# Optimization experiments

Measured on AMD Instinct MI355X. Metric: run time of the kernel, lower is better.

## Reference

```python
import jax, jax.numpy as jnp
import numpy as np

NUM_HEADS = 16
EMBED_DIM = 2048
HEAD_DIM = EMBED_DIM // NUM_HEADS
B, S = 2, 2048


def setup_inputs() -> dict:
    key = jax.random.key(0)
    ks = jax.random.split(key, 12)
    E = EMBED_DIM
    scale = 1.0 / np.sqrt(E)  # xavier-ish for square E->E dense
    inp = {
        "x": jax.random.normal(ks[0], (B, S, E), dtype=jnp.float32),
        "sin": jax.random.uniform(ks[1], (1, NUM_HEADS, S, HEAD_DIM), dtype=jnp.float32),
        "cos": jax.random.uniform(ks[2], (1, NUM_HEADS, S, HEAD_DIM), dtype=jnp.float32),
        "mask": jax.random.randint(ks[3], (B, S, S), 0, 2, dtype=jnp.int32),
        "Wq": jax.random.normal(ks[4], (E, E), dtype=jnp.float32) * scale,
        "bq": jnp.zeros((E,), dtype=jnp.float32),
        "Wk": jax.random.normal(ks[5], (E, E), dtype=jnp.float32) * scale,
        "bk": jnp.zeros((E,), dtype=jnp.float32),
        "Wv": jax.random.normal(ks[6], (E, E), dtype=jnp.float32) * scale,
        "bv": jnp.zeros((E,), dtype=jnp.float32),
        "Wo": jax.random.normal(ks[7], (E, E), dtype=jnp.float32) * scale,
        "bo": jnp.zeros((E,), dtype=jnp.float32),
    }
    return inp


def _minus_swap_alternate(t):
    # stack([-t[...,1::2], t[...,::2]], -1).reshape(t.shape)
    return jnp.stack([-t[..., 1::2], t[..., ::2]], axis=-1).reshape(t.shape)


def _forward(x, sin, cos, mask, Wq, bq, Wk, bk, Wv, bv, Wo, bo):
    Bx, Sx, E = x.shape
    H, D = NUM_HEADS, HEAD_DIM
    q = (x @ Wq + bq).reshape(Bx, Sx, H, D).transpose(0, 2, 1, 3)  # (B,H,S,D)
    k = (x @ Wk + bk).reshape(Bx, Sx, H, D).transpose(0, 2, 1, 3)
    v = (x @ Wv + bv).reshape(Bx, Sx, H, D).transpose(0, 2, 1, 3)
    # RoPE applied post-transpose: T = q.shape[1] == H (faithful to source)
    T = q.shape[1]
    s = sin[:, :T, :, :]
    c = cos[:, :T, :, :]
    q = q * c + _minus_swap_alternate(q) * s
    k = k * c + _minus_swap_alternate(k) * s
    m = mask[:, None, :, :]  # expand_mask: (B,S,S) -> (B,1,S,S)
    logits = jnp.einsum("bhqd,bhkd->bhqk", q, k) / jnp.sqrt(jnp.float32(D))
    logits = jnp.where(m == 0, jnp.float32(-9e15), logits)
    attention = jax.nn.softmax(logits, axis=-1)          # first softmax
    values = jnp.matmul(attention, v)                    # (B,H,S,D)
    attention_weights = jax.nn.softmax(attention, axis=-1)  # redundant second softmax
    attn_output = jnp.matmul(attention_weights, values)  # (B,H,S,D)
    attn_output = attn_output.transpose(0, 2, 1, 3).reshape(Bx, Sx, E)
    out = attn_output @ Wo + bo
    return out, attention_weights


def reference(x, sin, cos, mask, Wq, bq, Wk, bk, Wv, bv, Wo, bo):
    return _forward(x, sin, cos, mask, Wq, bq, Wk, bk, Wv, bv, Wo, bo)
```

## Files before the change

kernel.cpp:

```cpp
#include <hip/hip_runtime.h>

typedef unsigned short u16;
typedef unsigned int u32;
typedef __attribute__((ext_vector_type(8))) short short8;
typedef __attribute__((ext_vector_type(4))) float floatx4;

constexpr int Bc = 2, Sc = 2048, Ec = 2048, Hc = 16, Dc = 128;
constexpr int TILE = 128, BK = 64;

__device__ __forceinline__ u16 f2bf(float f) {
  u32 u = __builtin_bit_cast(u32, f);
  u = (u + 0x7FFFu + ((u >> 16) & 1u)) >> 16;
  return (u16)u;
}

__device__ __forceinline__ float bf2f(short s) {
  u32 u = ((u32)(u16)s) << 16;
  return __builtin_bit_cast(float, u);
}

__device__ __forceinline__ short8 pack2(float4 a, float4 b) {
  short8 r;
  r[0] = (short)f2bf(a.x); r[1] = (short)f2bf(a.y);
  r[2] = (short)f2bf(a.z); r[3] = (short)f2bf(a.w);
  r[4] = (short)f2bf(b.x); r[5] = (short)f2bf(b.y);
  r[6] = (short)f2bf(b.z); r[7] = (short)f2bf(b.w);
  return r;
}

__device__ __forceinline__ void glds16(const u16* g, u16* l) {
  __builtin_amdgcn_global_load_lds(
      (const __attribute__((address_space(1))) u32*)g,
      (__attribute__((address_space(3))) u32*)l, 16, 0, 0);
}

__device__ __forceinline__ void gemm_core(const u16* __restrict__ A, int lda,
                                          const u16* __restrict__ Bt, int ldb,
                                          int K, int m0, int n0,
                                          u16* smA, u16* smB,
                                          floatx4 (*acc)[4]) {
  const int t = threadIdx.x;
  const int lane = t & 63;
  const int w = t >> 6;
  const int wr = (w >> 1) * 64, wc = (w & 1) * 64;
  const int l15 = lane & 15, q = lane >> 4;

  const int r0 = t >> 3;
  const int c0 = (t & 7) ^ (r0 & 7);
  const u16* Ap = A + (size_t)(m0 + r0) * lda + c0 * 8;
  const u16* Bp = Bt + (size_t)(n0 + r0) * ldb + c0 * 8;
  u16* dA = smA + w * 512;
  u16* dB = smB + w * 512;

  for (int k0 = 0; k0 < K; k0 += BK) {
    #pragma unroll
    for (int j = 0; j < 4; j++) {
      glds16(Ap + (size_t)(32 * j) * lda + k0, dA + j * 2048);
      glds16(Bp + (size_t)(32 * j) * ldb + k0, dB + j * 2048);
    }
    __syncthreads();

    #pragma unroll
    for (int ks = 0; ks < 2; ks++) {
      short8 af[4], bfr[4];
      #pragma unroll
      for (int i = 0; i < 4; i++) {
        int ra = wr + i * 16 + l15;
        af[i] = *(const short8*)&smA[ra * BK + (((ks * 4 + q) ^ (ra & 7)) << 3)];
        int rb = wc + i * 16 + l15;
        bfr[i] = *(const short8*)&smB[rb * BK + (((ks * 4 + q) ^ (rb & 7)) << 3)];
      }
      #pragma unroll
      for (int mi = 0; mi < 4; mi++)
        #pragma unroll
        for (int ni = 0; ni < 4; ni++)
          acc[mi][ni] = __builtin_amdgcn_mfma_f32_16x16x32_bf16(af[mi], bfr[ni], acc[mi][ni], 0, 0, 0);
    }
    __syncthreads();
  }
}

__global__ __launch_bounds__(256) void transpose_w(
    const float* __restrict__ Wq, const float* __restrict__ Wk,
    const float* __restrict__ Wv, const float* __restrict__ Wo,
    u16* __restrict__ WT, u16* __restrict__ WoT) {
  __shared__ float tile[32][33];
  const int z = blockIdx.z;
  const float* W = (z == 0) ? Wq : (z == 1) ? Wk : (z == 2) ? Wv : Wo;
  u16* dst = (z < 3) ? (WT + (size_t)z * Ec * Ec) : WoT;
  const int n0 = blockIdx.x * 32, k0 = blockIdx.y * 32;
  const int tx = threadIdx.x, ty = threadIdx.y;
  #pragma unroll
  for (int i = 0; i < 4; i++)
    tile[ty + 8 * i][tx] = W[(size_t)(k0 + ty + 8 * i) * Ec + n0 + tx];
  __syncthreads();
  #pragma unroll
  for (int i = 0; i < 4; i++)
    dst[(size_t)(n0 + ty + 8 * i) * Ec + k0 + tx] = f2bf(tile[tx][ty + 8 * i]);
}

__global__ __launch_bounds__(256) void xcvt_kernel(const float* __restrict__ x,
                                                   u16* __restrict__ xb,
                                                   float* __restrict__ s1) {
  const int i = blockIdx.x * 256 + threadIdx.x;
  const float4 f0 = ((const float4*)x)[(size_t)i * 2];
  const float4 f1 = ((const float4*)x)[(size_t)i * 2 + 1];
  *(short8*)&xb[(size_t)i * 8] = pack2(f0, f1);
  if (blockIdx.x < 64)
    ((float4*)s1)[i] = make_float4(0.f, 0.f, 0.f, 0.f);
}

__global__ __launch_bounds__(256) void qkv_kernel(
    const u16* __restrict__ xb, const u16* __restrict__ WT,
    const float* __restrict__ bq, const float* __restrict__ bk, const float* __restrict__ bv,
    const float* __restrict__ sinp, const float* __restrict__ cosp,
    u16* __restrict__ qr, u16* __restrict__ kr, u16* __restrict__ vT) {
  __shared__ __align__(16) u16 smA[TILE * BK];
  __shared__ __align__(16) u16 smB[TILE * BK];
  floatx4 acc[4][4] = {};
  const int lin = blockIdx.y * 48 + blockIdx.x;
  const int swz = (lin & 7) * 192 + (lin >> 3);
  const int m0 = (swz / 48) * TILE, n0 = (swz % 48) * TILE;
  gemm_core(xb, Ec, WT, Ec, Ec, m0, n0, smA, smB, acc);

  const int t = threadIdx.x, lane = t & 63, w = t >> 6;
  const int wr = (w >> 1) * 64, wc = (w & 1) * 64, l15 = lane & 15, q = lane >> 4;
  #pragma unroll
  for (int mi = 0; mi < 4; mi++) {
    #pragma unroll
    for (int ni = 0; ni < 4; ni++) {
      const int gcol = n0 + wc + ni * 16 + l15;
      const int which = gcol >> 11;
      const int e = gcol & 2047, h = e >> 7, d = e & 127;
      const float* bp = (which == 0) ? bq : (which == 1) ? bk : bv;
      const float bias = bp[e];
      #pragma unroll
      for (int rr = 0; rr < 4; rr++) {
        const int grow = m0 + wr + mi * 16 + q * 4 + rr;
        const int b = grow >> 11, s = grow & 2047;
        float val = acc[mi][ni][rr] + bias;
        float pv = __shfl_xor(val, 1);
        if (which < 2) {
          const size_t sc = ((size_t)h * Sc + s) * Dc + d;
          const float c = cosp[sc], sn = sinp[sc];
          const float o = val * c + ((d & 1) ? pv : -pv) * sn;
          u16* dst = which ? kr : qr;
          dst[(((size_t)b * Hc + h) * Sc + s) * Dc + d] = f2bf(o);
        } else {
          vT[(((size_t)b * Hc + h) * Dc + d) * Sc + s] = f2bf(val);
        }
      }
    }
  }
}

__global__ __launch_bounds__(256) void logits_kernel(
    const u16* __restrict__ qr, const u16* __restrict__ kr,
    const int* __restrict__ maskp, u16* __restrict__ Pbuf, float* __restrict__ s1) {
  __shared__ __align__(16) u16 smA[TILE * BK];
  __shared__ __align__(16) u16 smB[TILE * BK];
  floatx4 acc[4][4] = {};
  const int z = blockIdx.z;
  const int m0 = blockIdx.y * TILE, n0 = blockIdx.x * TILE;
  gemm_core(qr + (size_t)z * Sc * Dc, Dc, kr + (size_t)z * Sc * Dc, Dc, Dc, m0, n0, smA, smB, acc);

  u16* Pp = Pbuf + (size_t)z * Sc * Sc;
  const int b = z >> 4;
  const float scale = 0.08838834764831845f;
  const int t = threadIdx.x, lane = t & 63, w = t >> 6;
  const int wr = (w >> 1) * 64, wc = (w & 1) * 64, l15 = lane & 15, q = lane >> 4;
  float rs[4][4];
  #pragma unroll
  for (int mi = 0; mi < 4; mi++)
    #pragma unroll
    for (int rr = 0; rr < 4; rr++) rs[mi][rr] = 0.f;

  #pragma unroll
  for (int mi = 0; mi < 4; mi++)
    #pragma unroll
    for (int ni = 0; ni < 4; ni++) {
      const int gcol = n0 + wc + ni * 16 + l15;
      #pragma unroll
      for (int rr = 0; rr < 4; rr++) {
        const int grow = m0 + wr + mi * 16 + q * 4 + rr;
        const int mv = maskp[((size_t)b * Sc + grow) * Sc + gcol];
        const float val = mv ? acc[mi][ni][rr] * scale : -9.0e15f;
        const float pe = __expf(val);
        rs[mi][rr] += pe;
        Pp[(size_t)grow * Sc + gcol] = f2bf(pe);
      }
    }
  #pragma unroll
  for (int mi = 0; mi < 4; mi++)
    #pragma unroll
    for (int rr = 0; rr < 4; rr++) {
      float xs = rs[mi][rr];
      xs += __shfl_xor(xs, 1);
      xs += __shfl_xor(xs, 2);
      xs += __shfl_xor(xs, 4);
      xs += __shfl_xor(xs, 8);
      if (l15 == 0)
        atomicAdd(&s1[z * Sc + m0 + wr + mi * 16 + q * 4 + rr], xs);
    }
}

__global__ __launch_bounds__(256) void av_kernel(
    const u16* __restrict__ P, const u16* __restrict__ vT,
    const float* __restrict__ s1, u16* __restrict__ valT, float* __restrict__ s2) {
  __shared__ __align__(16) u16 smA[64 * BK];
  __shared__ __align__(16) u16 smB[128 * BK];
  floatx4 acc[4][2] = {};
  const int z = blockIdx.z;
  const int m0 = blockIdx.y * 64;
  const int t = threadIdx.x, lane = t & 63, w = t >> 6;
  const int wc = w * 32;
  const int l15 = lane & 15, q = lane >> 4;

  const int r0 = t >> 3;
  const int c0 = (t & 7) ^ (r0 & 7);
  const u16* Pb = P + (size_t)z * Sc * Sc;
  const u16* Ap = Pb + (size_t)(m0 + r0) * Sc + c0 * 8;
  const u16* Bp = vT + (size_t)z * Dc * Sc + (size_t)r0 * Sc + c0 * 8;
  u16* dA = smA + w * 512;
  u16* dB = smB + w * 512;

  const float inv1a = 1.0f / s1[z * Sc + m0 + r0];
  const float inv1b = 1.0f / s1[z * Sc + m0 + r0 + 32];
  float s2a = 0.0f, s2b = 0.0f;

  for (int k0 = 0; k0 < Sc; k0 += BK) {
    glds16(Ap + k0, dA);
    glds16(Ap + (size_t)32 * Sc + k0, dA + 2048);
    #pragma unroll
    for (int j = 0; j < 4; j++)
      glds16(Bp + (size_t)(32 * j) * Sc + k0, dB + j * 2048);
    __syncthreads();

    short8 pa = *(const short8*)&smA[t * 8];
    short8 pb = *(const short8*)&smA[t * 8 + 2048];

    #pragma unroll
    for (int ks = 0; ks < 2; ks++) {
      short8 af[4], bfr[2];
      #pragma unroll
      for (int i = 0; i < 4; i++) {
        int ra = i * 16 + l15;
        af[i] = *(const short8*)&smA[ra * BK + (((ks * 4 + q) ^ (ra & 7)) << 3)];
      }
      #pragma unroll
      for (int i = 0; i < 2; i++) {
        int rb = wc + i * 16 + l15;
        bfr[i] = *(const short8*)&smB[rb * BK + (((ks * 4 + q) ^ (rb & 7)) << 3)];
      }
      #pragma unroll
      for (int mi = 0; mi < 4; mi++)
        #pragma unroll
        for (int ni = 0; ni < 2; ni++)
          acc[mi][ni] = __builtin_amdgcn_mfma_f32_16x16x32_bf16(af[mi], bfr[ni], acc[mi][ni], 0, 0, 0);
    }

    #pragma unroll
    for (int j = 0; j < 8; j++) {
      s2a += __expf(bf2f(pa[j]) * inv1a);
      s2b += __expf(bf2f(pb[j]) * inv1b);
    }
    __syncthreads();
  }

  s2a += __shfl_xor(s2a, 1); s2a += __shfl_xor(s2a, 2); s2a += __shfl_xor(s2a, 4);
  s2b += __shfl_xor(s2b, 1); s2b += __shfl_xor(s2b, 2); s2b += __shfl_xor(s2b, 4);
  if ((t & 7) == 0) {
    s2[z * Sc + m0 + r0] = s2a;
    s2[z * Sc + m0 + r0 + 32] = s2b;
  }

  float iv[4][4];
  #pragma unroll
  for (int mi = 0; mi < 4; mi++)
    #pragma unroll
    for (int rr = 0; rr < 4; rr++)
      iv[mi][rr] = 1.0f / s1[z * Sc + m0 + mi * 16 + q * 4 + rr];

  u16* C = valT + (size_t)z * Dc * Sc;
  #pragma unroll
  for (int mi = 0; mi < 4; mi++)
    #pragma unroll
    for (int ni = 0; ni < 2; ni++) {
      const int gcol = wc + ni * 16 + l15;
      #pragma unroll
      for (int rr = 0; rr < 4; rr++) {
        const int grow = m0 + mi * 16 + q * 4 + rr;
        C[(size_t)gcol * Sc + grow] = f2bf(acc[mi][ni][rr] * iv[mi][rr]);
      }
    }
}

__global__ __launch_bounds__(256) void wv_kernel(
    const u16* __restrict__ P, const u16* __restrict__ valT,
    const float* __restrict__ s1, const float* __restrict__ s2,
    float* __restrict__ a2out, u16* __restrict__ aox) {
  __shared__ __align__(16) u16 smA[64 * BK];
  __shared__ __align__(16) u16 smB[128 * BK];
  floatx4 acc[4][2] = {};
  const int z = blockIdx.z;
  const int m0 = blockIdx.y * 64;
  const int t = threadIdx.x, lane = t & 63, w = t >> 6;
  const int wc = w * 32;
  const int l15 = lane & 15, q = lane >> 4;

  const int r = t >> 2;
  const int cg2 = (t & 3) * 2;
  const int r0b = t >> 3;
  const int c0b = (t & 7) ^ (r0b & 7);
  const u16* Bp = valT + (size_t)z * Dc * Sc + (size_t)r0b * Sc + c0b * 8;
  u16* dB = smB + w * 512;

  const u16* Prow = P + (size_t)z * Sc * Sc + (size_t)(m0 + r) * Sc + cg2 * 8;
  float* Orow = a2out + (size_t)z * Sc * Sc + (size_t)(m0 + r) * Sc + cg2 * 8;
  const float inv1 = 1.0f / s1[z * Sc + m0 + r];
  const float inv2 = 1.0f / s2[z * Sc + m0 + r];

  for (int k0 = 0; k0 < Sc; k0 += BK) {
    #pragma unroll
    for (int j = 0; j < 4; j++)
      glds16(Bp + (size_t)(32 * j) * Sc + k0, dB + j * 2048);

    short8 p0 = *(const short8*)(Prow + k0);
    short8 p1 = *(const short8*)(Prow + k0 + 8);
    float4 f[4];
    float* e = (float*)f;
    #pragma unroll
    for (int j = 0; j < 8; j++) e[j] = __expf(bf2f(p0[j]) * inv1) * inv2;
    #pragma unroll
    for (int j = 0; j < 8; j++) e[8 + j] = __expf(bf2f(p1[j]) * inv1) * inv2;
    #pragma unroll
    for (int j = 0; j < 4; j++) ((float4*)(Orow + k0))[j] = f[j];
    short8 a0 = pack2(f[0], f[1]);
    short8 a1v = pack2(f[2], f[3]);
    *(short8*)&smA[r * BK + (((cg2 + 0) ^ (r & 7)) << 3)] = a0;
    *(short8*)&smA[r * BK + (((cg2 + 1) ^ (r & 7)) << 3)] = a1v;
    __syncthreads();

    #pragma unroll
    for (int ks = 0; ks < 2; ks++) {
      short8 af[4], bfr[2];
      #pragma unroll
      for (int i = 0; i < 4; i++) {
        int ra = i * 16 + l15;
        af[i] = *(const short8*)&smA[ra * BK + (((ks * 4 + q) ^ (ra & 7)) << 3)];
      }
      #pragma unroll
      for (int i = 0; i < 2; i++) {
        int rb = wc + i * 16 + l15;
        bfr[i] = *(const short8*)&smB[rb * BK + (((ks * 4 + q) ^ (rb & 7)) << 3)];
      }
      #pragma unroll
      for (int mi = 0; mi < 4; mi++)
        #pragma unroll
        for (int ni = 0; ni < 2; ni++)
          acc[mi][ni] = __builtin_amdgcn_mfma_f32_16x16x32_bf16(af[mi], bfr[ni], acc[mi][ni], 0, 0, 0);
    }
    __syncthreads();
  }

  const int b = z >> 4, h = z & 15;
  #pragma unroll
  for (int mi = 0; mi < 4; mi++)
    #pragma unroll
    for (int ni = 0; ni < 2; ni++) {
      const int gcol = wc + ni * 16 + l15;
      #pragma unroll
      for (int rr = 0; rr < 4; rr++) {
        const int grow = m0 + mi * 16 + q * 4 + rr;
        aox[((size_t)b * Sc + grow) * Ec + h * Dc + gcol] = f2bf(acc[mi][ni][rr]);
      }
    }
}

__global__ __launch_bounds__(256) void out_kernel(
    const u16* __restrict__ aox, const u16* __restrict__ WoT,
    const float* __restrict__ bo, float* __restrict__ outp) {
  __shared__ __align__(16) u16 smA[TILE * BK];
  __shared__ __align__(16) u16 smB[TILE * BK];
  floatx4 acc[4][4] = {};
  const int lin = blockIdx.y * 16 + blockIdx.x;
  const int swz = (lin & 7) * 64 + (lin >> 3);
  const int m0 = (swz / 16) * TILE, n0 = (swz % 16) * TILE;
  gemm_core(aox, Ec, WoT, Ec, Ec, m0, n0, smA, smB, acc);

  const int t = threadIdx.x, lane = t & 63, w = t >> 6;
  const int wr = (w >> 1) * 64, wc = (w & 1) * 64, l15 = lane & 15, q = lane >> 4;
  #pragma unroll
  for (int mi = 0; mi < 4; mi++)
    #pragma unroll
    for (int ni = 0; ni < 4; ni++) {
      const int gcol = n0 + wc + ni * 16 + l15;
      const float bias = bo[gcol];
      #pragma unroll
      for (int rr = 0; rr < 4; rr++) {
        const int grow = m0 + wr + mi * 16 + q * 4 + rr;
        outp[(size_t)grow * Ec + gcol] = acc[mi][ni][rr] + bias;
      }
    }
}

extern "C" void kernel_launch(void* const* d_in, const int* in_sizes, int n_in,
                              void* d_out, int out_size, void* d_ws, size_t ws_size,
                              hipStream_t stream) {
  const float* x     = (const float*)d_in[0];
  const float* sinp  = (const float*)d_in[1];
  const float* cosp  = (const float*)d_in[2];
  const int*   maskp = (const int*)d_in[3];
  const float* Wq    = (const float*)d_in[4];
  const float* bq    = (const float*)d_in[5];
  const float* Wk    = (const float*)d_in[6];
  const float* bk    = (const float*)d_in[7];
  const float* Wv    = (const float*)d_in[8];
  const float* bv    = (const float*)d_in[9];
  const float* Wo    = (const float*)d_in[10];
  const float* bo    = (const float*)d_in[11];

  float* out0  = (float*)d_out;
  float* attnL = out0 + (size_t)Bc * Sc * Ec;

  u16* wsp  = (u16*)d_ws;
  u16* WT   = wsp;
  u16* WoT  = WT + (size_t)3 * Ec * Ec;
  u16* xb   = WoT + (size_t)Ec * Ec;
  u16* qr   = xb + (size_t)Bc * Sc * Ec;
  u16* kr   = qr + (size_t)Bc * Hc * Sc * Dc;
  u16* vT   = kr + (size_t)Bc * Hc * Sc * Dc;
  u16* valT = vT + (size_t)Bc * Hc * Sc * Dc;
  u16* aox  = valT + (size_t)Bc * Hc * Sc * Dc;
  float* s1 = (float*)(aox + (size_t)Bc * Sc * Ec);
  float* s2 = s1 + (size_t)Bc * Hc * Sc;
  u16* Pbuf = (u16*)(s2 + (size_t)Bc * Hc * Sc);

  transpose_w<<<dim3(64, 64, 4), dim3(32, 8), 0, stream>>>(Wq, Wk, Wv, Wo, WT, WoT);
  xcvt_kernel<<<dim3(4096), 256, 0, stream>>>(x, xb, s1);
  qkv_kernel<<<dim3(48, 32), 256, 0, stream>>>(xb, WT, bq, bk, bv, sinp, cosp, qr, kr, vT);
  logits_kernel<<<dim3(16, 16, 32), 256, 0, stream>>>(qr, kr, maskp, Pbuf, s1);
  av_kernel<<<dim3(1, 32, 32), 256, 0, stream>>>(Pbuf, vT, s1, valT, s2);
  wv_kernel<<<dim3(1, 32, 32), 256, 0, stream>>>(Pbuf, valT, s1, s2, attnL, aox);
  out_kernel<<<dim3(16, 32), 256, 0, stream>>>(aox, WoT, bo, out0);
}
```

Baseline: 1.298 ms.

## Fuse logits and attention-value kernels, bit-pack mask, move second-softmax sum into wv

Merges the QK^T logits kernel and the P·V kernel into one flash-style kernel. Each block keeps Q fragments in registers and streams K and V tiles, computing exp(logits), writing P to global memory and accumulating P·V. The int32 mask is packed into a bitmask during the x conversion so the fused kernel reads 1 bit per entry instead of 4 bytes. The second softmax row sum moves into wv_kernel as an extra pass over P. This removes one full re-read of P and the atomics on s1, at the cost of fewer blocks (512) and more registers per thread in the fused kernel.

Result: slower. 1.539 ms (+18.5%).

```diff
diff --git a/kernel.cpp b/kernel.cpp
--- a/kernel.cpp
+++ b/kernel.cpp
@@ -101,13 +101,28 @@
 
 __global__ __launch_bounds__(256) void xcvt_kernel(const float* __restrict__ x,
                                                    u16* __restrict__ xb,
-                                                   float* __restrict__ s1) {
+                                                   float* __restrict__ s1,
+                                                   const int* __restrict__ mp,
+                                                   u32* __restrict__ mb) {
   const int i = blockIdx.x * 256 + threadIdx.x;
   const float4 f0 = ((const float4*)x)[(size_t)i * 2];
   const float4 f1 = ((const float4*)x)[(size_t)i * 2 + 1];
   *(short8*)&xb[(size_t)i * 8] = pack2(f0, f1);
   if (blockIdx.x < 64)
     ((float4*)s1)[i] = make_float4(0.f, 0.f, 0.f, 0.f);
+  if (blockIdx.x < 1024) {
+    const int4* src = (const int4*)mp + (size_t)i * 8;
+    u32 wv = 0;
+    #pragma unroll
+    for (int j = 0; j < 8; j++) {
+      const int4 v = src[j];
+      wv |= (u32)(v.x != 0) << (j * 4 + 0);
+      wv |= (u32)(v.y != 0) << (j * 4 + 1);
+      wv |= (u32)(v.z != 0) << (j * 4 + 2);
+      wv |= (u32)(v.w != 0) << (j * 4 + 3);
+    }
+    mb[i] = wv;
+  }
 }
 
 __global__ __launch_bounds__(256) void qkv_kernel(
@@ -154,42 +169,127 @@
   }
 }
 
-__global__ __launch_bounds__(256) void logits_kernel(
-    const u16* __restrict__ qr, const u16* __restrict__ kr,
-    const int* __restrict__ maskp, u16* __restrict__ Pbuf, float* __restrict__ s1) {
-  __shared__ __align__(16) u16 smA[TILE * BK];
-  __shared__ __align__(16) u16 smB[TILE * BK];
-  floatx4 acc[4][4] = {};
+__global__ __launch_bounds__(256) void lav_kernel(
+    const u16* __restrict__ qr, const u16* __restrict__ kr, const u16* __restrict__ vT,
+    const u32* __restrict__ mb, u16* __restrict__ Pbuf,
+    float* __restrict__ s1, u16* __restrict__ valT) {
+  __shared__ __align__(16) u16 sm[24576];
+  u16* smK = sm;
+  u16* smV = sm + 8192;
+  u16* smP = sm + 16384;
+
   const int z = blockIdx.z;
-  const int m0 = blockIdx.y * TILE, n0 = blockIdx.x * TILE;
-  gemm_core(qr + (size_t)z * Sc * Dc, Dc, kr + (size_t)z * Sc * Dc, Dc, Dc, m0, n0, smA, smB, acc);
-
-  u16* Pp = Pbuf + (size_t)z * Sc * Sc;
+  const int m0 = blockIdx.y * 128;
+  const int t = threadIdx.x, lane = t & 63, w = t >> 6;
+  const int wr = (w >> 1) * 64;
+  const int wcS = (w & 1) * 32;
+  const int wcU = (w & 1) * 64;
+  const int l15 = lane & 15, q = lane >> 4;
   const int b = z >> 4;
   const float scale = 0.08838834764831845f;
-  const int t = threadIdx.x, lane = t & 63, w = t >> 6;
-  const int wr = (w >> 1) * 64, wc = (w & 1) * 64, l15 = lane & 15, q = lane >> 4;
+
+  const u16* qh = qr + (size_t)z * Sc * Dc;
+  const u16* kh = kr + (size_t)z * Sc * Dc;
+  const u16* vh = vT + (size_t)z * Dc * Sc;
+  u16* Pp = Pbuf + (size_t)z * Sc * Sc;
+
+  short8 Qf[4][4];
+  #pragma unroll
+  for (int mi = 0; mi < 4; mi++)
+    #pragma unroll
+    for (int es = 0; es < 4; es++)
+      Qf[mi][es] = *(const short8*)&qh[(size_t)(m0 + wr + mi * 16 + l15) * Dc + (es * 4 + q) * 8];
+
+  floatx4 Uacc[4][4] = {};
   float rs[4][4];
   #pragma unroll
   for (int mi = 0; mi < 4; mi++)
     #pragma unroll
     for (int rr = 0; rr < 4; rr++) rs[mi][rr] = 0.f;
 
-  #pragma unroll
-  for (int mi = 0; mi < 4; mi++)
+  const int rK = t >> 4;
+  const int cK = (t & 15) ^ ((t >> 4) & 15);
+  const u16* Ksrc = kh + (size_t)rK * Dc + cK * 8;
+  const int rV = t >> 3;
+  const int cV = (t & 7) ^ (rV & 7);
+  const u16* Vsrc = vh + (size_t)rV * Sc + cV * 8;
+  u16* dK = smK + w * 512;
+  u16* dV = smV + w * 512;
+
+  for (int kt = 0; kt < 32; kt++) {
+    const int kb = kt * 64;
+    #pragma unroll
+    for (int j = 0; j < 4; j++) {
+      glds16(Ksrc + (size_t)(kb + 16 * j) * Dc, dK + j * 2048);
+      glds16(Vsrc + (size_t)(32 * j) * Sc + kb, dV + j * 2048);
+    }
+    __syncthreads();
+
+    floatx4 Sacc[4][2] = {};
+    short8 Kf[2][4];
+    #pragma unroll
+    for (int ni = 0; ni < 2; ni++) {
+      const int rb = wcS + ni * 16 + l15;
+      #pragma unroll
+      for (int es = 0; es < 4; es++)
+        Kf[ni][es] = *(const short8*)&smK[rb * 128 + (((es * 4 + q) ^ (rb & 15)) << 3)];
+    }
+    #pragma unroll
+    for (int mi = 0; mi < 4; mi++)
+      #pragma unroll
+      for (int ni = 0; ni < 2; ni++)
+        #pragma unroll
+        for (int es = 0; es < 4; es++)
+          Sacc[mi][ni] = __builtin_amdgcn_mfma_f32_16x16x32_bf16(Qf[mi][es], Kf[ni][es], Sacc[mi][ni], 0, 0, 0);
+
+    #pragma unroll
+    for (int mi = 0; mi < 4; mi++)
+      #pragma unroll
+      for (int rr = 0; rr < 4; rr++) {
+        const int sr = wr + mi * 16 + q * 4 + rr;
+        const int srg = m0 + sr;
+        const u32* mrow = mb + ((size_t)b * Sc + srg) * (Sc / 32);
+        #pragma unroll
+        for (int ni = 0; ni < 2; ni++) {
+          const int kc = wcS + ni * 16 + l15;
+          const int kg = kb + kc;
+          const u32 mw = mrow[kg >> 5];
+          const float val = ((mw >> (kg & 31)) & 1) ? Sacc[mi][ni][rr] * scale : -9.0e15f;
+          const float pe = __expf(val);
+          rs[mi][rr] += pe;
+          const u16 pb = f2bf(pe);
+          smP[sr * 64 + ((((kc >> 3) ^ (sr & 7)) << 3) | (kc & 7))] = pb;
+          Pp[(size_t)srg * Sc + kg] = pb;
+        }
+      }
+    __syncthreads();
+
+    short8 Pf[4][2], Vf[4][2];
+    #pragma unroll
+    for (int mi = 0; mi < 4; mi++) {
+      const int ar = wr + mi * 16 + l15;
+      #pragma unroll
+      for (int ks = 0; ks < 2; ks++)
+        Pf[mi][ks] = *(const short8*)&smP[ar * 64 + (((ks * 4 + q) ^ (ar & 7)) << 3)];
+    }
     #pragma unroll
     for (int ni = 0; ni < 4; ni++) {
-      const int gcol = n0 + wc + ni * 16 + l15;
-      #pragma unroll
-      for (int rr = 0; rr < 4; rr++) {
-        const int grow = m0 + wr + mi * 16 + q * 4 + rr;
-        const int mv = maskp[((size_t)b * Sc + grow) * Sc + gcol];
-        const float val = mv ? acc[mi][ni][rr] * scale : -9.0e15f;
-        const float pe = __expf(val);
-        rs[mi][rr] += pe;
-        Pp[(size_t)grow * Sc + gcol] = f2bf(pe);
-      }
-    }
+      const int rb = wcU + ni * 16 + l15;
+      #pragma unroll
+      for (int ks = 0; ks < 2; ks++)
+        Vf[ni][ks] = *(const short8*)&smV[rb * 64 + (((ks * 4 + q) ^ (rb & 7)) << 3)];
+    }
+    #pragma unroll
+    for (int mi = 0; mi < 4; mi++)
+      #pragma unroll
+      for (int ni = 0; ni < 4; ni++)
+        #pragma unroll
+        for (int ks = 0; ks < 2; ks++)
+          Uacc[mi][ni] = __builtin_amdgcn_mfma_f32_16x16x32_bf16(Pf[mi][ks], Vf[ni][ks], Uacc[mi][ni], 0, 0, 0);
+    __syncthreads();
+  }
+
+  float* redp = (float*)sm;
   #pragma unroll
   for (int mi = 0; mi < 4; mi++)
     #pragma unroll
@@ -199,16 +299,47 @@
       xs += __shfl_xor(xs, 2);
       xs += __shfl_xor(xs, 4);
       xs += __shfl_xor(xs, 8);
-      if (l15 == 0)
-        atomicAdd(&s1[z * Sc + m0 + wr + mi * 16 + q * 4 + rr], xs);
-    }
-}
-
-__global__ __launch_bounds__(256) void av_kernel(
-    const u16* __restrict__ P, const u16* __restrict__ vT,
-    const float* __restrict__ s1, u16* __restrict__ valT, float* __restrict__ s2) {
+      if (l15 == 0) redp[(w & 1) * 128 + wr + mi * 16 + q * 4 + rr] = xs;
+    }
+  __syncthreads();
+  if (t < 128) {
+    const float v = redp[t] + redp[128 + t];
+    s1[z * Sc + m0 + t] = v;
+    redp[256 + t] = v;
+  }
+  __syncthreads();
+
+  u16* smT = sm + 8192;
+  #pragma unroll
+  for (int mi = 0; mi < 4; mi++)
+    #pragma unroll
+    for (int ni = 0; ni < 4; ni++) {
+      const int d = wcU + ni * 16 + l15;
+      #pragma unroll
+      for (int rr = 0; rr < 4; rr++) {
+        const int i = wr + mi * 16 + q * 4 + rr;
+        const float val = Uacc[mi][ni][rr] / redp[256 + i];
+        smT[d * 128 + ((((i >> 3) ^ (d & 7)) << 3) | (i & 7))] = f2bf(val);
+      }
+    }
+  __syncthreads();
+  u16* C = valT + (size_t)z * Dc * Sc;
+  const int dd = t >> 1, half = (t & 1) * 8;
+  #pragma unroll
+  for (int j = 0; j < 8; j++) {
+    const int cj = half + j;
+    *(short8*)&C[(size_t)dd * Sc + m0 + cj * 8] =
+        *(const short8*)&smT[dd * 128 + ((cj ^ (dd & 7)) << 3)];
+  }
+}
+
+__global__ __launch_bounds__(256) void wv_kernel(
+    const u16* __restrict__ P, const u16* __restrict__ valT,
+    const float* __restrict__ s1,
+    float* __restrict__ a2out, u16* __restrict__ aox) {
   __shared__ __align__(16) u16 smA[64 * BK];
   __shared__ __align__(16) u16 smB[128 * BK];
+  __shared__ float s2row[64];
   floatx4 acc[4][2] = {};
   const int z = blockIdx.z;
   const int m0 = blockIdx.y * 64;
@@ -216,99 +347,24 @@
   const int wc = w * 32;
   const int l15 = lane & 15, q = lane >> 4;
 
-  const int r0 = t >> 3;
-  const int c0 = (t & 7) ^ (r0 & 7);
-  const u16* Pb = P + (size_t)z * Sc * Sc;
-  const u16* Ap = Pb + (size_t)(m0 + r0) * Sc + c0 * 8;
-  const u16* Bp = vT + (size_t)z * Dc * Sc + (size_t)r0 * Sc + c0 * 8;
-  u16* dA = smA + w * 512;
-  u16* dB = smB + w * 512;
-
-  const float inv1a = 1.0f / s1[z * Sc + m0 + r0];
-  const float inv1b = 1.0f / s1[z * Sc + m0 + r0 + 32];
-  float s2a = 0.0f, s2b = 0.0f;
-
-  for (int k0 = 0; k0 < Sc; k0 += BK) {
-    glds16(Ap + k0, dA);
-    glds16(Ap + (size_t)32 * Sc + k0, dA + 2048);
-    #pragma unroll
-    for (int j = 0; j < 4; j++)
-      glds16(Bp + (size_t)(32 * j) * Sc + k0, dB + j * 2048);
-    __syncthreads();
-
-    short8 pa = *(const short8*)&smA[t * 8];
-    short8 pb = *(const short8*)&smA[t * 8 + 2048];
-
-    #pragma unroll
-    for (int ks = 0; ks < 2; ks++) {
-      short8 af[4], bfr[2];
-      #pragma unroll
-      for (int i = 0; i < 4; i++) {
-        int ra = i * 16 + l15;
-        af[i] = *(const short8*)&smA[ra * BK + (((ks * 4 + q) ^ (ra & 7)) << 3)];
-      }
-      #pragma unroll
-      for (int i = 0; i < 2; i++) {
-        int rb = wc + i * 16 + l15;
-        bfr[i] = *(const short8*)&smB[rb * BK + (((ks * 4 + q) ^ (rb & 7)) << 3)];
-      }
-      #pragma unroll
-      for (int mi = 0; mi < 4; mi++)
-        #pragma unroll
-        for (int ni = 0; ni < 2; ni++)
-          acc[mi][ni] = __builtin_amdgcn_mfma_f32_16x16x32_bf16(af[mi], bfr[ni], acc[mi][ni], 0, 0, 0);
-    }
-
-    #pragma unroll
-    for (int j = 0; j < 8; j++) {
-      s2a += __expf(bf2f(pa[j]) * inv1a);
-      s2b += __expf(bf2f(pb[j]) * inv1b);
-    }
-    __syncthreads();
-  }
-
-  s2a += __shfl_xor(s2a, 1); s2a += __shfl_xor(s2a, 2); s2a += __shfl_xor(s2a, 4);
-  s2b += __shfl_xor(s2b, 1); s2b += __shfl_xor(s2b, 2); s2b += __shfl_xor(s2b, 4);
-  if ((t & 7) == 0) {
-    s2[z * Sc + m0 + r0] = s2a;
-    s2[z * Sc + m0 + r0 + 32] = s2b;
-  }
-
-  float iv[4][4];
-  #pragma unroll
-  for (int mi = 0; mi < 4; mi++)
-    #pragma unroll
-    for (int rr = 0; rr < 4; rr++)
-      iv[mi][rr] = 1.0f / s1[z * Sc + m0 + mi * 16 + q * 4 + rr];
-
-  u16* C = valT + (size_t)z * Dc * Sc;
-  #pragma unroll
-  for (int mi = 0; mi < 4; mi++)
-    #pragma unroll
-    for (int ni = 0; ni < 2; ni++) {
-      const int gcol = wc + ni * 16 + l15;
-      #pragma unroll
-      for (int rr = 0; rr < 4; rr++) {
-        const int grow = m0 + mi * 16 + q * 4 + rr;
-        C[(size_t)gcol * Sc + grow] = f2bf(acc[mi][ni][rr] * iv[mi][rr]);
-      }
-    }
-}
-
-__global__ __launch_bounds__(256) void wv_kernel(
-    const u16* __restrict__ P, const u16* __restrict__ valT,
-    const float* __restrict__ s1, const float* __restrict__ s2,
-    float* __restrict__ a2out, u16* __restrict__ aox) {
-  __shared__ __align__(16) u16 smA[64 * BK];
-  __shared__ __align__(16) u16 smB[128 * BK];
-  floatx4 acc[4][2] = {};
-  const int z = blockIdx.z;
-  const int m0 = blockIdx.y * 64;
-  const int t = threadIdx.x, lane = t & 63, w = t >> 6;
-  const int wc = w * 32;
-  const int l15 = lane & 15, q = lane >> 4;
-
   const int r = t >> 2;
+  const float inv1 = 1.0f / s1[z * Sc + m0 + r];
+
+  {
+    const u16* Pr0 = P + (size_t)z * Sc * Sc + (size_t)(m0 + r) * Sc + (t & 3) * 512;
+    float ps2 = 0.f;
+    for (int c = 0; c < 512; c += 8) {
+      short8 pv = *(const short8*)&Pr0[c];
+      #pragma unroll
+      for (int j = 0; j < 8; j++) ps2 += __expf(bf2f(pv[j]) * inv1);
+    }
+    ps2 += __shfl_xor(ps2, 1);
+    ps2 += __shfl_xor(ps2, 2);
+    if ((t & 3) == 0) s2row[r] = ps2;
+  }
+  __syncthreads();
+  const float inv2 = 1.0f / s2row[r];
+
   const int cg2 = (t & 3) * 2;
   const int r0b = t >> 3;
   const int c0b = (t & 7) ^ (r0b & 7);
@@ -317,8 +373,6 @@
 
   const u16* Prow = P + (size_t)z * Sc * Sc + (size_t)(m0 + r) * Sc + cg2 * 8;
   float* Orow = a2out + (size_t)z * Sc * Sc + (size_t)(m0 + r) * Sc + cg2 * 8;
-  const float inv1 = 1.0f / s1[z * Sc + m0 + r];
-  const float inv2 = 1.0f / s2[z * Sc + m0 + r];
 
   for (int k0 = 0; k0 < Sc; k0 += BK) {
     #pragma unroll
@@ -435,12 +489,12 @@
   float* s1 = (float*)(aox + (size_t)Bc * Sc * Ec);
   float* s2 = s1 + (size_t)Bc * Hc * Sc;
   u16* Pbuf = (u16*)(s2 + (size_t)Bc * Hc * Sc);
+  u32* mb   = (u32*)(Pbuf + (size_t)Bc * Hc * Sc * Sc);
 
   transpose_w<<<dim3(64, 64, 4), dim3(32, 8), 0, stream>>>(Wq, Wk, Wv, Wo, WT, WoT);
-  xcvt_kernel<<<dim3(4096), 256, 0, stream>>>(x, xb, s1);
+  xcvt_kernel<<<dim3(4096), 256, 0, stream>>>(x, xb, s1, maskp, mb);
   qkv_kernel<<<dim3(48, 32), 256, 0, stream>>>(xb, WT, bq, bk, bv, sinp, cosp, qr, kr, vT);
-  logits_kernel<<<dim3(16, 16, 32), 256, 0, stream>>>(qr, kr, maskp, Pbuf, s1);
-  av_kernel<<<dim3(1, 32, 32), 256, 0, stream>>>(Pbuf, vT, s1, valT, s2);
-  wv_kernel<<<dim3(1, 32, 32), 256, 0, stream>>>(Pbuf, valT, s1, s2, attnL, aox);
+  lav_kernel<<<dim3(1, 16, 32), 256, 0, stream>>>(qr, kr, vT, mb, Pbuf, s1, valT);
+  wv_kernel<<<dim3(1, 32, 32), 256, 0, stream>>>(Pbuf, valT, s1, attnL, aox);
   out_kernel<<<dim3(16, 32), 256, 0, stream>>>(aox, WoT, bo, out0);
 }
```
